# Kernel tuning notes

Measured on AMD Instinct MI355X. Metric: run time of the kernel, lower is better.

## Reference

```python
import jax, jax.numpy as jnp
import numpy as np

HIDDEN = 128
EDGE = 64
EPS = 1e-5

def setup_inputs() -> dict:
    key = jax.random.key(0)
    ks = jax.random.split(key, 12)
    B, N, D = 8, 256, HIDDEN
    h = jax.random.normal(ks[0], (B, N, D), dtype=jnp.float32)
    edge_feats = jax.random.normal(ks[1], (B, N, N, 3), dtype=jnp.float32)
    adj_mask = jax.random.bernoulli(ks[2], 0.5, (B, N, N))
    s = lambda fan_in: 1.0 / np.sqrt(fan_in)
    W1 = jax.random.uniform(ks[3], (D + 3, EDGE), minval=-s(D + 3), maxval=s(D + 3))
    b1 = jnp.zeros((EDGE,), jnp.float32)
    W2 = jax.random.uniform(ks[4], (EDGE, D), minval=-s(EDGE), maxval=s(EDGE))
    b2 = jnp.zeros((D,), jnp.float32)
    U1 = jax.random.uniform(ks[5], (3 * D, D), minval=-s(3 * D), maxval=s(3 * D))
    b3 = jnp.zeros((D,), jnp.float32)
    U2 = jax.random.uniform(ks[6], (D, D), minval=-s(D), maxval=s(D))
    b4 = jnp.zeros((D,), jnp.float32)
    gamma = jnp.ones((D,), jnp.float32)
    beta = jnp.zeros((D,), jnp.float32)
    return {"h": h, "edge_feats": edge_feats, "adj_mask": adj_mask,
            "W1": W1, "b1": b1, "W2": W2, "b2": b2,
            "U1": U1, "b3": b3, "U2": U2, "b4": b4,
            "gamma": gamma, "beta": beta}

def reference(h, edge_feats, adj_mask, W1, b1, W2, b2, U1, b3, U2, b4, gamma, beta):
    B, N, D = h.shape
    # NOTE: torch does h.unsqueeze(2).expand(B,N,N,D): h_j[b,i,j,:] = h[b,i,:]
    h_j = jnp.broadcast_to(h[:, :, None, :], (B, N, N, D))
    gate_in = jnp.concatenate([h_j, edge_feats], axis=-1)          # (B,N,N,D+3)
    gates = jax.nn.sigmoid(jax.nn.relu(gate_in @ W1 + b1) @ W2 + b2)  # (B,N,N,D)
    mask_f = adj_mask.astype(h.dtype)[..., None]                    # (B,N,N,1)
    messages = gates * h_j * mask_f
    neighbor_count = jnp.clip(jnp.sum(mask_f, axis=2), 1.0)         # (B,N,1)
    agg_mean = jnp.sum(messages, axis=2) / neighbor_count           # (B,N,D)
    msgs_max = jnp.where(adj_mask[..., None], messages, -jnp.inf)
    agg_max = jnp.max(msgs_max, axis=2)
    agg_max = jnp.where(jnp.isinf(agg_max), 0.0, agg_max)
    upd_in = jnp.concatenate([h, agg_mean, agg_max], axis=-1)       # (B,N,3D)
    upd = jax.nn.relu(upd_in @ U1 + b3) @ U2 + b4
    x = h + upd
    mu = jnp.mean(x, axis=-1, keepdims=True)
    var = jnp.var(x, axis=-1, keepdims=True)
    return (x - mu) * jax.lax.rsqrt(var + EPS) * gamma + beta
```

## Files before the change

### kernel.cpp

```cpp
#include <hip/hip_runtime.h>
#include <hip/hip_bf16.h>
#include <math.h>

#define NN 256
#define DD 128
#define EE 64
#define APAD 392
#define RPAD 136

typedef __attribute__((ext_vector_type(8))) short short8;
typedef __attribute__((ext_vector_type(4))) float f32x4;

static __device__ __forceinline__ unsigned short f2bf(float f) {
    __hip_bfloat16 b = __float2bfloat16(f);
    return *reinterpret_cast<unsigned short*>(&b);
}

static __device__ __forceinline__ float sigm(float l) {
    return __fdividef(1.f, 1.f + __expf(-l));
}

static __device__ __forceinline__ short8 ldb(const float* __restrict__ B, int kbase, int d) {
    unsigned short tmp[8];
    #pragma unroll
    for (int j = 0; j < 8; ++j) tmp[j] = f2bf(B[(kbase + j) * DD + d]);
    return *(const short8*)tmp;
}

__global__ __launch_bounds__(256, 4)
void ecgc_gate(const float* __restrict__ h_g,
               const float* __restrict__ ef_g,
               const int*   __restrict__ mask_g,
               const float* __restrict__ W1_g,
               const float* __restrict__ b1_g,
               const float* __restrict__ W2_g,
               const float* __restrict__ b2_g,
               const float* __restrict__ U1_g,
               const float* __restrict__ U2_g,
               float*          __restrict__ aggf,
               unsigned short* __restrict__ u1t,
               unsigned short* __restrict__ u2t)
{
    const int bi   = blockIdx.x;
    const int t    = threadIdx.x;
    const int lane = t & 63;
    const int w    = t >> 6;
    const int m16  = lane & 15;
    const int quad = lane >> 4;

    __shared__ __align__(16) float sh_ef4[NN * 4];
    __shared__ __align__(16) float sh_q4[EE * 4];
    __shared__ float sh_basep[4 * EE];
    __shared__ float sh_w1e[3 * EE];
    __shared__ int   sh_jlist[NN], sh_wcnt[4], sh_cnt;

    if (t < 32) {
        const int flat = bi * 32 + t;
        if (flat < 384 * DD) {
            const int d = flat / 384, k = flat - d * 384;
            u1t[flat] = f2bf(U1_g[k * DD + d]);
        } else {
            const int f2i = flat - 384 * DD;
            const int d = f2i >> 7, k = f2i & 127;
            u2t[f2i] = f2bf(U2_g[k * DD + d]);
        }
    }

    {
        const float* efr = ef_g + (size_t)bi * NN * 3;
        sh_ef4[t * 4 + 0] = efr[t * 3 + 0];
        sh_ef4[t * 4 + 1] = efr[t * 3 + 1];
        sh_ef4[t * 4 + 2] = efr[t * 3 + 2];
        sh_ef4[t * 4 + 3] = 0.f;
    }
    if (t < 192) sh_w1e[t] = W1_g[(DD + (t >> 6)) * EE + (t & 63)];

    const int mk = (mask_g[bi * NN + t] != 0) ? 1 : 0;
    const unsigned long long bal = __ballot(mk);
    if (lane == 0) sh_wcnt[w] = __popcll(bal);
    const int pre = __popcll(bal & ((1ull << lane) - 1ull));

    {
        const int e = t & 63;
        float acc = 0.f;
        #pragma unroll 8
        for (int d = w * 32; d < w * 32 + 32; ++d)
            acc = fmaf(h_g[bi * DD + d], W1_g[d * EE + e], acc);
        sh_basep[w * EE + e] = acc;
    }

    const int dstripe = w * 32;
    short8 bfrag[2][2];
    float  nb2[2], hd2[2], flip[2];
    #pragma unroll
    for (int dt = 0; dt < 2; ++dt) {
        const int d = dstripe + 16 * dt + m16;
        nb2[dt] = b2_g[d];
        hd2[dt] = h_g[bi * DD + d];
        flip[dt] = (hd2[dt] >= 0.f) ? 1.f : -1.f;
        #pragma unroll
        for (int kh = 0; kh < 2; ++kh)
            bfrag[dt][kh] = ldb(W2_g, kh * 32 + quad * 8, d);
    }
    __syncthreads();

    {
        int wbase = 0;
        for (int ww = 0; ww < w; ++ww) wbase += sh_wcnt[ww];
        if (mk) sh_jlist[wbase + pre] = t;
        if (t == 0) sh_cnt = sh_wcnt[0] + sh_wcnt[1] + sh_wcnt[2] + sh_wcnt[3];
    }
    if (t < EE) {
        const float base = b1_g[t] + sh_basep[t] + sh_basep[EE + t] +
                           sh_basep[2 * EE + t] + sh_basep[3 * EE + t];
        sh_q4[t * 4 + 0] = base;
        sh_q4[t * 4 + 1] = sh_w1e[t];
        sh_q4[t * 4 + 2] = sh_w1e[EE + t];
        sh_q4[t * 4 + 3] = sh_w1e[2 * EE + t];
    }
    __syncthreads();

    f32x4 qa[8], qb[8];
    #pragma unroll
    for (int jj = 0; jj < 8; ++jj) {
        qa[jj] = *(const f32x4*)&sh_q4[(quad * 8 + jj) * 4];
        qb[jj] = *(const f32x4*)&sh_q4[(32 + quad * 8 + jj) * 4];
    }

    const int cnt = sh_cnt;
    const int njt = (cnt + 15) >> 4;

    float sum2[2] = {0.f, 0.f};
    float mm[2]   = {-3.0e38f, -3.0e38f};

    for (int jt = 0; jt < njt; ++jt) {
        const int row = jt * 16 + m16;
        int jl = sh_jlist[row];
        jl = (row < cnt) ? jl : 0;
        const float4 efv = *(const float4*)&sh_ef4[jl * 4];

        union { short8 s; __hip_bfloat162 h2[4]; } ua, ub;
        #pragma unroll
        for (int p = 0; p < 4; ++p) {
            const f32x4 qa0 = qa[2 * p], qa1 = qa[2 * p + 1];
            const f32x4 qb0 = qb[2 * p], qb1 = qb[2 * p + 1];
            float2 va, vb;
            va.x = fmaxf(fmaf(efv.z, qa0[3], fmaf(efv.y, qa0[2], fmaf(efv.x, qa0[1], qa0[0]))), 0.f);
            va.y = fmaxf(fmaf(efv.z, qa1[3], fmaf(efv.y, qa1[2], fmaf(efv.x, qa1[1], qa1[0]))), 0.f);
            vb.x = fmaxf(fmaf(efv.z, qb0[3], fmaf(efv.y, qb0[2], fmaf(efv.x, qb0[1], qb0[0]))), 0.f);
            vb.y = fmaxf(fmaf(efv.z, qb1[3], fmaf(efv.y, qb1[2], fmaf(efv.x, qb1[1], qb1[0]))), 0.f);
            ua.h2[p] = __float22bfloat162_rn(va);
            ub.h2[p] = __float22bfloat162_rn(vb);
        }

        const bool tail = (jt == njt - 1) && (cnt & 15);
        #pragma unroll
        for (int dt = 0; dt < 2; ++dt) {
            f32x4 acc = {nb2[dt], nb2[dt], nb2[dt], nb2[dt]};
            acc = __builtin_amdgcn_mfma_f32_16x16x32_bf16(ua.s, bfrag[dt][0], acc, 0, 0, 0);
            acc = __builtin_amdgcn_mfma_f32_16x16x32_bf16(ub.s, bfrag[dt][1], acc, 0, 0, 0);
            if (!tail) {
                #pragma unroll
                for (int r = 0; r < 4; ++r) {
                    const float l = acc[r];
                    mm[dt] = fmaxf(mm[dt], l * flip[dt]);
                    sum2[dt] += sigm(l);
                }
            } else {
                #pragma unroll
                for (int r = 0; r < 4; ++r) {
                    const bool v = (jt * 16 + quad * 4 + r) < cnt;
                    const float lx = v ? acc[r] : -3.0e38f;
                    const float pf = v ? acc[r] * flip[dt] : -3.0e38f;
                    mm[dt] = fmaxf(mm[dt], pf);
                    sum2[dt] += sigm(lx);
                }
            }
        }
    }

    #pragma unroll
    for (int dt = 0; dt < 2; ++dt) {
        float s = sum2[dt], M = mm[dt];
        s += __shfl_xor(s, 16, 64);  s += __shfl_xor(s, 32, 64);
        M  = fmaxf(M,  __shfl_xor(M, 16, 64));  M  = fmaxf(M,  __shfl_xor(M, 32, 64));
        if (quad == 0) {
            const int d = dstripe + 16 * dt + m16;
            const float hd = hd2[dt];
            float mean = 0.f, amax = 0.f;
            if (cnt > 0) {
                mean = hd * s * __fdividef(1.f, (float)cnt);
                amax = hd * sigm(flip[dt] * M);
            }
            aggf[bi * 256 + d]       = mean;
            aggf[bi * 256 + 128 + d] = amax;
        }
    }
}

__global__ __launch_bounds__(256, 2)
void ecgc_upd(const float* __restrict__ h_g,
              const float* __restrict__ aggf,
              const unsigned short* __restrict__ u1t,
              const unsigned short* __restrict__ u2t,
              const float* __restrict__ b3_g,
              const float* __restrict__ b4_g,
              const float* __restrict__ gam_g,
              const float* __restrict__ bet_g,
              float*       __restrict__ out_g)
{
    const int bi0  = blockIdx.x * 16;
    const int t    = threadIdx.x;
    const int lane = t & 63;
    const int w    = t >> 6;
    const int m16  = lane & 15;
    const int quad = lane >> 4;

    __shared__ __align__(16) unsigned short shA[16 * APAD];
    __shared__ __align__(16) unsigned short rbuf[16 * RPAD];
    __shared__ float sh_s[4 * 16], sh_s2[4 * 16], sh_mu[16], sh_rs[16];

    {
        const int row = t >> 4, q = t & 15;
        const float* hrow = h_g  + (size_t)(bi0 + row) * DD;
        const float* wrow = aggf + (size_t)(bi0 + row) * 256;
        unsigned short tmp[24];
        #pragma unroll
        for (int c = 0; c < 24; ++c) {
            const int col = q * 24 + c;
            float v;
            if (col < 128)      v = hrow[col];
            else if (col < 256) v = wrow[col - 128];
            else                v = wrow[col - 256 + 128];
            tmp[c] = f2bf(v);
        }
        #pragma unroll
        for (int s8 = 0; s8 < 3; ++s8)
            *(short8*)&shA[row * APAD + q * 24 + s8 * 8] = *(const short8*)&tmp[s8 * 8];
    }
    __syncthreads();

    const int dstripe = w * 32;

    f32x4 acc[2];
    #pragma unroll
    for (int dt = 0; dt < 2; ++dt) {
        const float bb = b3_g[dstripe + dt * 16 + m16];
        acc[dt] = (f32x4){bb, bb, bb, bb};
    }
    for (int kk = 0; kk < 12; ++kk) {
        const short8 a0 = *(const short8*)&shA[m16 * APAD + kk * 32 + quad * 8];
        #pragma unroll
        for (int dt = 0; dt < 2; ++dt) {
            const int d = dstripe + dt * 16 + m16;
            const short8 b = *(const short8*)&u1t[(size_t)d * 384 + kk * 32 + quad * 8];
            acc[dt] = __builtin_amdgcn_mfma_f32_16x16x32_bf16(a0, b, acc[dt], 0, 0, 0);
        }
    }

    #pragma unroll
    for (int dt = 0; dt < 2; ++dt) {
        const int d = dstripe + dt * 16 + m16;
        #pragma unroll
        for (int r = 0; r < 4; ++r) {
            const int ro = quad * 4 + r;
            rbuf[ro * RPAD + d] = f2bf(fmaxf(acc[dt][r], 0.f));
        }
    }
    __syncthreads();

    f32x4 acc2[2];
    #pragma unroll
    for (int dt = 0; dt < 2; ++dt) {
        const float bb = b4_g[dstripe + dt * 16 + m16];
        acc2[dt] = (f32x4){bb, bb, bb, bb};
    }
    for (int kk = 0; kk < 4; ++kk) {
        const short8 a0 = *(const short8*)&rbuf[m16 * RPAD + kk * 32 + quad * 8];
        #pragma unroll
        for (int dt = 0; dt < 2; ++dt) {
            const int d = dstripe + dt * 16 + m16;
            const short8 b = *(const short8*)&u2t[(size_t)d * 128 + kk * 32 + quad * 8];
            acc2[dt] = __builtin_amdgcn_mfma_f32_16x16x32_bf16(a0, b, acc2[dt], 0, 0, 0);
        }
    }

    float xv[2][4];
    #pragma unroll
    for (int dt = 0; dt < 2; ++dt) {
        const int d = dstripe + dt * 16 + m16;
        #pragma unroll
        for (int r = 0; r < 4; ++r) {
            const int ro = quad * 4 + r;
            xv[dt][r] = h_g[(size_t)(bi0 + ro) * DD + d] + acc2[dt][r];
        }
    }

    #pragma unroll
    for (int r = 0; r < 4; ++r) {
        float s  = xv[0][r] + xv[1][r];
        float s2 = xv[0][r] * xv[0][r] + xv[1][r] * xv[1][r];
        #pragma unroll
        for (int off = 1; off < 16; off <<= 1) {
            s  += __shfl_xor(s,  off, 64);
            s2 += __shfl_xor(s2, off, 64);
        }
        if (m16 == 0) {
            const int ro = quad * 4 + r;
            sh_s[w * 16 + ro]  = s;
            sh_s2[w * 16 + ro] = s2;
        }
    }
    __syncthreads();
    if (t < 16) {
        const float S  = sh_s[t]  + sh_s[16 + t]  + sh_s[32 + t]  + sh_s[48 + t];
        const float S2 = sh_s2[t] + sh_s2[16 + t] + sh_s2[32 + t] + sh_s2[48 + t];
        const float mu  = S * (1.f / 128.f);
        const float var = S2 * (1.f / 128.f) - mu * mu;
        sh_mu[t] = mu;
        sh_rs[t] = rsqrtf(var + 1e-5f);
    }
    __syncthreads();

    #pragma unroll
    for (int dt = 0; dt < 2; ++dt) {
        const int d = dstripe + dt * 16 + m16;
        const float ga = gam_g[d], be = bet_g[d];
        #pragma unroll
        for (int r = 0; r < 4; ++r) {
            const int ro = quad * 4 + r;
            out_g[(size_t)(bi0 + ro) * DD + d] =
                (xv[dt][r] - sh_mu[ro]) * sh_rs[ro] * ga + be;
        }
    }
}

extern "C" void kernel_launch(void* const* d_in, const int* in_sizes, int n_in,
                              void* d_out, int out_size, void* d_ws, size_t ws_size,
                              hipStream_t stream) {
    float* aggf = (float*)d_ws;
    unsigned short* u1t = (unsigned short*)((char*)d_ws + (size_t)2048 * 256 * 4);
    unsigned short* u2t = u1t + 384 * DD;
    ecgc_gate<<<8 * NN, 256, 0, stream>>>(
        (const float*)d_in[0],
        (const float*)d_in[1],
        (const int*)d_in[2],
        (const float*)d_in[3],
        (const float*)d_in[4],
        (const float*)d_in[5],
        (const float*)d_in[6],
        (const float*)d_in[7],
        (const float*)d_in[9],
        aggf, u1t, u2t);
    ecgc_upd<<<(8 * NN) / 16, 256, 0, stream>>>(
        (const float*)d_in[0],
        aggf, u1t, u2t,
        (const float*)d_in[8],
        (const float*)d_in[10],
        (const float*)d_in[11],
        (const float*)d_in[12],
        (float*)d_out);
}
```

Measured before the change: 121.2 us.

## Share hidden-layer tile via swizzled double-buffered LDS and retile U1/U2 layout

The edge-MLP first layer was computed redundantly: each of the 4 waves built the full 16x64 bf16 A fragment from per-edge features. Now each thread computes only 4 hidden units for one row, writes them into a swizzled, double-buffered LDS tile, and all waves read their MFMA A fragments from it. This adds a block-wide barrier per j-tile. Separately, the transposed U1/U2 bf16 copies are stored in a k-chunked [k/8][d][8] layout so the update-MLP B-fragment loads are contiguous across lanes.

```diff
diff --git a/kernel.cpp b/kernel.cpp
--- a/kernel.cpp
+++ b/kernel.cpp
@@ -47,22 +47,25 @@
     const int w    = t >> 6;
     const int m16  = lane & 15;
     const int quad = lane >> 4;
+    const int bj   = t & 15;
+    const int beb  = (t >> 4) << 2;
 
     __shared__ __align__(16) float sh_ef4[NN * 4];
     __shared__ __align__(16) float sh_q4[EE * 4];
     __shared__ float sh_basep[4 * EE];
     __shared__ float sh_w1e[3 * EE];
     __shared__ int   sh_jlist[NN], sh_wcnt[4], sh_cnt;
+    __shared__ __align__(16) unsigned short sh_P[2][16 * EE];
 
     if (t < 32) {
         const int flat = bi * 32 + t;
         if (flat < 384 * DD) {
             const int d = flat / 384, k = flat - d * 384;
-            u1t[flat] = f2bf(U1_g[k * DD + d]);
+            u1t[((k >> 3) * DD + d) * 8 + (k & 7)] = f2bf(U1_g[k * DD + d]);
         } else {
             const int f2i = flat - 384 * DD;
             const int d = f2i >> 7, k = f2i & 127;
-            u2t[f2i] = f2bf(U2_g[k * DD + d]);
+            u2t[((k >> 3) * DD + d) * 8 + (k & 7)] = f2bf(U2_g[k * DD + d]);
         }
     }
 
@@ -120,45 +123,59 @@
     }
     __syncthreads();
 
-    f32x4 qa[8], qb[8];
-    #pragma unroll
-    for (int jj = 0; jj < 8; ++jj) {
-        qa[jj] = *(const f32x4*)&sh_q4[(quad * 8 + jj) * 4];
-        qb[jj] = *(const f32x4*)&sh_q4[(32 + quad * 8 + jj) * 4];
-    }
+    f32x4 qreg[4];
+    #pragma unroll
+    for (int i = 0; i < 4; ++i) qreg[i] = *(const f32x4*)&sh_q4[(beb + i) * 4];
 
     const int cnt = sh_cnt;
     const int njt = (cnt + 15) >> 4;
 
+    const int   sw_r = (m16 & 7) << 4;
+    const char* prow = (const char*)&sh_P[0][m16 * EE];
+    const int   offA = (quad * 16) ^ sw_r;
+    const int   offB = (64 + quad * 16) ^ sw_r;
+    char* pwr;
+    {
+        const int cb = 2 * beb;
+        const int cs = (cb & 8) | ((((cb >> 4) ^ (bj & 7)) & 7) << 4);
+        pwr = (char*)&sh_P[0][bj * EE] + cs;
+    }
+
     float sum2[2] = {0.f, 0.f};
     float mm[2]   = {-3.0e38f, -3.0e38f};
 
-    for (int jt = 0; jt < njt; ++jt) {
-        const int row = jt * 16 + m16;
+    auto buildP = [&](int jtile, int bufbyte) {
+        const int row = jtile * 16 + bj;
         int jl = sh_jlist[row];
         jl = (row < cnt) ? jl : 0;
         const float4 efv = *(const float4*)&sh_ef4[jl * 4];
-
-        union { short8 s; __hip_bfloat162 h2[4]; } ua, ub;
-        #pragma unroll
-        for (int p = 0; p < 4; ++p) {
-            const f32x4 qa0 = qa[2 * p], qa1 = qa[2 * p + 1];
-            const f32x4 qb0 = qb[2 * p], qb1 = qb[2 * p + 1];
-            float2 va, vb;
-            va.x = fmaxf(fmaf(efv.z, qa0[3], fmaf(efv.y, qa0[2], fmaf(efv.x, qa0[1], qa0[0]))), 0.f);
-            va.y = fmaxf(fmaf(efv.z, qa1[3], fmaf(efv.y, qa1[2], fmaf(efv.x, qa1[1], qa1[0]))), 0.f);
-            vb.x = fmaxf(fmaf(efv.z, qb0[3], fmaf(efv.y, qb0[2], fmaf(efv.x, qb0[1], qb0[0]))), 0.f);
-            vb.y = fmaxf(fmaf(efv.z, qb1[3], fmaf(efv.y, qb1[2], fmaf(efv.x, qb1[1], qb1[0]))), 0.f);
-            ua.h2[p] = __float22bfloat162_rn(va);
-            ub.h2[p] = __float22bfloat162_rn(vb);
-        }
+        float v[4];
+        #pragma unroll
+        for (int i = 0; i < 4; ++i)
+            v[i] = fmaxf(fmaf(efv.z, qreg[i][3], fmaf(efv.y, qreg[i][2],
+                         fmaf(efv.x, qreg[i][1], qreg[i][0]))), 0.f);
+        union { __hip_bfloat162 h2; unsigned int u; } a0, a1;
+        a0.h2 = __float22bfloat162_rn(make_float2(v[0], v[1]));
+        a1.h2 = __float22bfloat162_rn(make_float2(v[2], v[3]));
+        *reinterpret_cast<uint2*>(pwr + bufbyte) = make_uint2(a0.u, a1.u);
+    };
+
+    if (njt > 0) buildP(0, 0);
+    __syncthreads();
+
+    for (int jt = 0; jt < njt; ++jt) {
+        const int bo = (jt & 1) << 11;
+        const short8 ua = *(const short8*)(prow + bo + offA);
+        const short8 ub = *(const short8*)(prow + bo + offB);
+
+        if (jt + 1 < njt) buildP(jt + 1, bo ^ 2048);
 
         const bool tail = (jt == njt - 1) && (cnt & 15);
         #pragma unroll
         for (int dt = 0; dt < 2; ++dt) {
             f32x4 acc = {nb2[dt], nb2[dt], nb2[dt], nb2[dt]};
-            acc = __builtin_amdgcn_mfma_f32_16x16x32_bf16(ua.s, bfrag[dt][0], acc, 0, 0, 0);
-            acc = __builtin_amdgcn_mfma_f32_16x16x32_bf16(ub.s, bfrag[dt][1], acc, 0, 0, 0);
+            acc = __builtin_amdgcn_mfma_f32_16x16x32_bf16(ua, bfrag[dt][0], acc, 0, 0, 0);
+            acc = __builtin_amdgcn_mfma_f32_16x16x32_bf16(ub, bfrag[dt][1], acc, 0, 0, 0);
             if (!tail) {
                 #pragma unroll
                 for (int r = 0; r < 4; ++r) {
@@ -177,6 +194,7 @@
                 }
             }
         }
+        __syncthreads();
     }
 
     #pragma unroll
@@ -253,7 +271,7 @@
         #pragma unroll
         for (int dt = 0; dt < 2; ++dt) {
             const int d = dstripe + dt * 16 + m16;
-            const short8 b = *(const short8*)&u1t[(size_t)d * 384 + kk * 32 + quad * 8];
+            const short8 b = *(const short8*)&u1t[(size_t)((kk * 4 + quad) * DD + d) * 8];
             acc[dt] = __builtin_amdgcn_mfma_f32_16x16x32_bf16(a0, b, acc[dt], 0, 0, 0);
         }
     }
@@ -280,7 +298,7 @@
         #pragma unroll
         for (int dt = 0; dt < 2; ++dt) {
             const int d = dstripe + dt * 16 + m16;
-            const short8 b = *(const short8*)&u2t[(size_t)d * 128 + kk * 32 + quad * 8];
+            const short8 b = *(const short8*)&u2t[(size_t)((kk * 4 + quad) * DD + d) * 8];
             acc2[dt] = __builtin_amdgcn_mfma_f32_16x16x32_bf16(a0, b, acc2[dt], 0, 0, 0);
         }
     }
```

Measured after the change: 116.0 us. -4.3%, faster.

## Split neighbor tiles across waves with full-D W2 in LDS; retile U1/U2 layout

Applied to the files above, without the earlier changes.

The gate kernel now splits the neighbor row tiles across the four waves, so each wave covers all 128 output channels instead of a fixed 32-channel stripe and the redundant per-wave first-layer recomputation goes away. To support this, W2 is staged once per block as bf16 MFMA fragments in shared memory, and the per-wave partial sums and maxima are reduced through shared memory at the end. The q coefficients are now read from swizzled LDS inside the loop instead of being held in registers. The transposed U1/U2 buffers are rewritten in a k-blocked layout so the update kernel's B-fragment loads are coalesced across lanes. The trade-offs are more LDS (16KB for W2), extra per-iteration LDS reads, eight accumulator sets, and an additional barrier for the reduction.

```diff
diff --git a/kernel.cpp b/kernel.cpp
--- a/kernel.cpp
+++ b/kernel.cpp
@@ -18,13 +18,6 @@
 
 static __device__ __forceinline__ float sigm(float l) {
     return __fdividef(1.f, 1.f + __expf(-l));
-}
-
-static __device__ __forceinline__ short8 ldb(const float* __restrict__ B, int kbase, int d) {
-    unsigned short tmp[8];
-    #pragma unroll
-    for (int j = 0; j < 8; ++j) tmp[j] = f2bf(B[(kbase + j) * DD + d]);
-    return *(const short8*)tmp;
 }
 
 __global__ __launch_bounds__(256, 4)
@@ -53,16 +46,18 @@
     __shared__ float sh_basep[4 * EE];
     __shared__ float sh_w1e[3 * EE];
     __shared__ int   sh_jlist[NN], sh_wcnt[4], sh_cnt;
+    __shared__ __align__(16) unsigned short sh_w2[8192];
+    __shared__ float sh_rsum[4 * DD], sh_rmax[4 * DD];
 
     if (t < 32) {
         const int flat = bi * 32 + t;
         if (flat < 384 * DD) {
             const int d = flat / 384, k = flat - d * 384;
-            u1t[flat] = f2bf(U1_g[k * DD + d]);
+            u1t[((k >> 3) * DD + d) * 8 + (k & 7)] = f2bf(U1_g[k * DD + d]);
         } else {
             const int f2i = flat - 384 * DD;
             const int d = f2i >> 7, k = f2i & 127;
-            u2t[f2i] = f2bf(U2_g[k * DD + d]);
+            u2t[((k >> 3) * DD + d) * 8 + (k & 7)] = f2bf(U2_g[k * DD + d]);
         }
     }
 
@@ -89,18 +84,29 @@
         sh_basep[w * EE + e] = acc;
     }
 
-    const int dstripe = w * 32;
-    short8 bfrag[2][2];
-    float  nb2[2], hd2[2], flip[2];
-    #pragma unroll
-    for (int dt = 0; dt < 2; ++dt) {
-        const int d = dstripe + 16 * dt + m16;
-        nb2[dt] = b2_g[d];
-        hd2[dt] = h_g[bi * DD + d];
-        flip[dt] = (hd2[dt] >= 0.f) ? 1.f : -1.f;
-        #pragma unroll
-        for (int kh = 0; kh < 2; ++kh)
-            bfrag[dt][kh] = ldb(W2_g, kh * 32 + quad * 8, d);
+    {
+        #pragma unroll
+        for (int s = 0; s < 4; ++s) {
+            const int c   = s * 256 + t;
+            const int cm  = c & 15;
+            const int cq  = (c >> 4) & 3;
+            const int ckh = (c >> 6) & 1;
+            const int cdt = c >> 7;
+            const int k0  = ckh * 32 + cq * 8;
+            const int d   = cdt * 16 + cm;
+            unsigned short tmp[8];
+            #pragma unroll
+            for (int jj = 0; jj < 8; ++jj) tmp[jj] = f2bf(W2_g[(k0 + jj) * DD + d]);
+            *(short8*)&sh_w2[c * 8] = *(const short8*)tmp;
+        }
+    }
+
+    float nb2[8], flip[8];
+    #pragma unroll
+    for (int dt = 0; dt < 8; ++dt) {
+        const int d = dt * 16 + m16;
+        nb2[dt]  = b2_g[d];
+        flip[dt] = (h_g[bi * DD + d] >= 0.f) ? 1.f : -1.f;
     }
     __syncthreads();
 
@@ -113,27 +119,22 @@
     if (t < EE) {
         const float base = b1_g[t] + sh_basep[t] + sh_basep[EE + t] +
                            sh_basep[2 * EE + t] + sh_basep[3 * EE + t];
-        sh_q4[t * 4 + 0] = base;
-        sh_q4[t * 4 + 1] = sh_w1e[t];
-        sh_q4[t * 4 + 2] = sh_w1e[EE + t];
-        sh_q4[t * 4 + 3] = sh_w1e[2 * EE + t];
-    }
-    __syncthreads();
-
-    f32x4 qa[8], qb[8];
-    #pragma unroll
-    for (int jj = 0; jj < 8; ++jj) {
-        qa[jj] = *(const f32x4*)&sh_q4[(quad * 8 + jj) * 4];
-        qb[jj] = *(const f32x4*)&sh_q4[(32 + quad * 8 + jj) * 4];
-    }
+        const int s = ((t & 7) << 3) | (t >> 3);
+        sh_q4[s * 4 + 0] = base;
+        sh_q4[s * 4 + 1] = sh_w1e[t];
+        sh_q4[s * 4 + 2] = sh_w1e[EE + t];
+        sh_q4[s * 4 + 3] = sh_w1e[2 * EE + t];
+    }
+    __syncthreads();
 
     const int cnt = sh_cnt;
     const int njt = (cnt + 15) >> 4;
 
-    float sum2[2] = {0.f, 0.f};
-    float mm[2]   = {-3.0e38f, -3.0e38f};
-
-    for (int jt = 0; jt < njt; ++jt) {
+    float sum2[8], mm[8];
+    #pragma unroll
+    for (int dt = 0; dt < 8; ++dt) { sum2[dt] = 0.f; mm[dt] = -3.0e38f; }
+
+    for (int jt = w; jt < njt; jt += 4) {
         const int row = jt * 16 + m16;
         int jl = sh_jlist[row];
         jl = (row < cnt) ? jl : 0;
@@ -142,8 +143,10 @@
         union { short8 s; __hip_bfloat162 h2[4]; } ua, ub;
         #pragma unroll
         for (int p = 0; p < 4; ++p) {
-            const f32x4 qa0 = qa[2 * p], qa1 = qa[2 * p + 1];
-            const f32x4 qb0 = qb[2 * p], qb1 = qb[2 * p + 1];
+            const f32x4 qa0 = *(const f32x4*)&sh_q4[((2*p    ) * 8 + quad) * 4];
+            const f32x4 qa1 = *(const f32x4*)&sh_q4[((2*p + 1) * 8 + quad) * 4];
+            const f32x4 qb0 = *(const f32x4*)&sh_q4[((2*p    ) * 8 + 4 + quad) * 4];
+            const f32x4 qb1 = *(const f32x4*)&sh_q4[((2*p + 1) * 8 + 4 + quad) * 4];
             float2 va, vb;
             va.x = fmaxf(fmaf(efv.z, qa0[3], fmaf(efv.y, qa0[2], fmaf(efv.x, qa0[1], qa0[0]))), 0.f);
             va.y = fmaxf(fmaf(efv.z, qa1[3], fmaf(efv.y, qa1[2], fmaf(efv.x, qa1[1], qa1[0]))), 0.f);
@@ -155,10 +158,13 @@
 
         const bool tail = (jt == njt - 1) && (cnt & 15);
         #pragma unroll
-        for (int dt = 0; dt < 2; ++dt) {
+        for (int dt = 0; dt < 8; ++dt) {
+            const int fb = ((dt * 8 + quad) * 16 + m16) * 8;
+            const short8 b0 = *(const short8*)&sh_w2[fb];
+            const short8 b1 = *(const short8*)&sh_w2[fb + 512];
             f32x4 acc = {nb2[dt], nb2[dt], nb2[dt], nb2[dt]};
-            acc = __builtin_amdgcn_mfma_f32_16x16x32_bf16(ua.s, bfrag[dt][0], acc, 0, 0, 0);
-            acc = __builtin_amdgcn_mfma_f32_16x16x32_bf16(ub.s, bfrag[dt][1], acc, 0, 0, 0);
+            acc = __builtin_amdgcn_mfma_f32_16x16x32_bf16(ua.s, b0, acc, 0, 0, 0);
+            acc = __builtin_amdgcn_mfma_f32_16x16x32_bf16(ub.s, b1, acc, 0, 0, 0);
             if (!tail) {
                 #pragma unroll
                 for (int r = 0; r < 4; ++r) {
@@ -180,21 +186,31 @@
     }
 
     #pragma unroll
-    for (int dt = 0; dt < 2; ++dt) {
+    for (int dt = 0; dt < 8; ++dt) {
         float s = sum2[dt], M = mm[dt];
         s += __shfl_xor(s, 16, 64);  s += __shfl_xor(s, 32, 64);
         M  = fmaxf(M,  __shfl_xor(M, 16, 64));  M  = fmaxf(M,  __shfl_xor(M, 32, 64));
         if (quad == 0) {
-            const int d = dstripe + 16 * dt + m16;
-            const float hd = hd2[dt];
-            float mean = 0.f, amax = 0.f;
-            if (cnt > 0) {
-                mean = hd * s * __fdividef(1.f, (float)cnt);
-                amax = hd * sigm(flip[dt] * M);
-            }
-            aggf[bi * 256 + d]       = mean;
-            aggf[bi * 256 + 128 + d] = amax;
-        }
+            sh_rsum[w * DD + dt * 16 + m16] = s;
+            sh_rmax[w * DD + dt * 16 + m16] = M;
+        }
+    }
+    __syncthreads();
+
+    if (t < DD) {
+        const int d = t;
+        const float S = sh_rsum[d] + sh_rsum[DD + d] + sh_rsum[2 * DD + d] + sh_rsum[3 * DD + d];
+        const float M = fmaxf(fmaxf(sh_rmax[d], sh_rmax[DD + d]),
+                              fmaxf(sh_rmax[2 * DD + d], sh_rmax[3 * DD + d]));
+        const float hd = h_g[bi * DD + d];
+        const float fl = (hd >= 0.f) ? 1.f : -1.f;
+        float mean = 0.f, amax = 0.f;
+        if (cnt > 0) {
+            mean = hd * S * __fdividef(1.f, (float)cnt);
+            amax = hd * sigm(fl * M);
+        }
+        aggf[bi * 256 + d]       = mean;
+        aggf[bi * 256 + 128 + d] = amax;
     }
 }
 
@@ -253,7 +269,7 @@
         #pragma unroll
         for (int dt = 0; dt < 2; ++dt) {
             const int d = dstripe + dt * 16 + m16;
-            const short8 b = *(const short8*)&u1t[(size_t)d * 384 + kk * 32 + quad * 8];
+            const short8 b = *(const short8*)&u1t[(size_t)((kk * 4 + quad) * DD + d) * 8];
             acc[dt] = __builtin_amdgcn_mfma_f32_16x16x32_bf16(a0, b, acc[dt], 0, 0, 0);
         }
     }
@@ -280,7 +296,7 @@
         #pragma unroll
         for (int dt = 0; dt < 2; ++dt) {
             const int d = dstripe + dt * 16 + m16;
-            const short8 b = *(const short8*)&u2t[(size_t)d * 128 + kk * 32 + quad * 8];
+            const short8 b = *(const short8*)&u2t[(size_t)((kk * 4 + quad) * DD + d) * 8];
             acc2[dt] = __builtin_amdgcn_mfma_f32_16x16x32_bf16(a0, b, acc2[dt], 0, 0, 0);
         }
     }
```

Measured after the change: 305.8 us. +152.4%, slower.
